# Optimization experiments

Hardware: AMD Instinct MI355X
Metric: run time of the kernel (lower is better)

## Reference

```python
import jax, jax.numpy as jnp
import numpy as np

DIM = 768
H = 12
HD = DIM // H
LAMBDA_INIT = 0.1
EPS = 1e-6


def setup_inputs() -> dict:
    key = jax.random.key(0)
    ks = jax.random.split(key, 6)
    B, N = 2, 2048
    x = jax.random.normal(ks[0], (B, N, DIM), dtype=jnp.float32)
    xpos = jnp.broadcast_to(jnp.arange(N, dtype=jnp.int64), (B, N))
    s = 1.0 / np.sqrt(DIM)
    W_qkv1 = jax.random.normal(ks[1], (DIM, 3 * DIM), dtype=jnp.float32) * s
    W_qkv2 = jax.random.normal(ks[2], (DIM, 3 * DIM), dtype=jnp.float32) * s
    W_proj = jax.random.normal(ks[3], (DIM, DIM), dtype=jnp.float32) * s
    b_proj = jnp.zeros((DIM,), dtype=jnp.float32)
    norm_w = jnp.ones((DIM,), dtype=jnp.float32)
    lambda_1 = jnp.ones((H,), dtype=jnp.float32)
    # layer_idx=0, max_layer=12 -> scale = 1/12
    lambda_2 = jnp.full((H,), 1.0 - LAMBDA_INIT * (1.0 / 12.0), dtype=jnp.float32)
    return {"x": x, "W_qkv1": W_qkv1, "W_qkv2": W_qkv2, "W_proj": W_proj,
            "b_proj": b_proj, "norm_w": norm_w, "lambda_1": lambda_1,
            "lambda_2": lambda_2, "xpos": xpos}


def _qkv(x, W):
    B, N, C = x.shape
    qkv = (x @ W).reshape(B, N, 3, H, HD).transpose(2, 0, 3, 1, 4)  # [3,B,H,N,D]
    return qkv[0], qkv[1], qkv[2]


def reference(x, W_qkv1, W_qkv2, W_proj, b_proj, norm_w, lambda_1, lambda_2, xpos):
    B, N, C = x.shape
    scale = HD ** -0.5
    q1, k1, v1 = _qkv(x, W_qkv1)
    q2, k2, v2 = _qkv(x, W_qkv2)
    attn1 = jax.nn.softmax(jnp.einsum('bhnd,bhmd->bhnm', q1, k1) * scale, axis=-1)
    attn2 = jax.nn.softmax(jnp.einsum('bhnd,bhmd->bhnm', q2, k2) * scale, axis=-1)
    lam = (lambda_1 - lambda_2 + LAMBDA_INIT)[None, :, None, None]
    diff_attn = attn1 - lam * attn2
    out = jnp.einsum('bhnm,bhmd->bhnd', diff_attn, v1)
    out = out.transpose(0, 2, 1, 3).reshape(B, N, C)
    # RMSNorm (computed in fp32, matching torch module)
    o32 = out.astype(jnp.float32)
    rms = jax.lax.rsqrt(jnp.mean(o32 * o32, axis=-1, keepdims=True) + EPS)
    out = (o32 * rms * norm_w).astype(out.dtype)
    return out @ W_proj + b_proj
```

## Files before the change

### kernel.cpp

```cpp
#include <hip/hip_runtime.h>
#include <hip/hip_bf16.h>
#include <math.h>

#define DIMC 768
#define NH   12
#define HDIM 64
#define NSEQ 2048
#define NB   2
#define LAMBDA_INIT 0.1f

typedef __attribute__((ext_vector_type(8))) short bf16x8;
typedef __attribute__((ext_vector_type(4))) float f32x4;
typedef unsigned short u16;

__device__ __forceinline__ u16 f2b(float f) {
    unsigned u = __float_as_uint(f);
    return (u16)((u + 0x7FFFu + ((u >> 16) & 1u)) >> 16);
}
__device__ __forceinline__ float b2f(u16 h) {
    return __uint_as_float((unsigned)h << 16);
}

__global__ __launch_bounds__(256)
void split32(const float* __restrict__ x, u16* __restrict__ hi,
             u16* __restrict__ lo, int n4)
{
    for (int i = blockIdx.x * 256 + threadIdx.x; i < n4; i += gridDim.x * 256) {
        float4 v = ((const float4*)x)[i];
        ushort4 h, l;
        h.x = f2b(v.x); l.x = f2b(v.x - b2f(h.x));
        h.y = f2b(v.y); l.y = f2b(v.y - b2f(h.y));
        h.z = f2b(v.z); l.z = f2b(v.z - b2f(h.z));
        h.w = f2b(v.w); l.w = f2b(v.w - b2f(h.w));
        ((ushort4*)hi)[i] = h;
        ((ushort4*)lo)[i] = l;
    }
}

__global__ __launch_bounds__(256)
void tsplit(const float* __restrict__ src, int R, int C_ld,
            u16* __restrict__ dhi, u16* __restrict__ dlo)
{
    __shared__ float T[64][65];
    const int tid = threadIdx.x;
    const int c0 = blockIdx.x * 64, r0 = blockIdx.y * 64;
    const int row = tid >> 2, cq = (tid & 3) * 4;
#pragma unroll
    for (int it = 0; it < 4; ++it) {
        int col = cq + it * 16;
        float4 v = *(const float4*)&src[(size_t)(r0 + row) * C_ld + c0 + col];
        T[row][col+0] = v.x; T[row][col+1] = v.y;
        T[row][col+2] = v.z; T[row][col+3] = v.w;
    }
    __syncthreads();
    const int c = tid >> 2, rq = (tid & 3) * 4;
#pragma unroll
    for (int it = 0; it < 4; ++it) {
        int rr = rq + it * 16;
#pragma unroll
        for (int i = 0; i < 4; ++i) {
            float f = T[rr + i][c];
            u16 h = f2b(f);
            size_t o = (size_t)(c0 + c) * R + r0 + rr + i;
            dhi[o] = h;
            dlo[o] = f2b(f - b2f(h));
        }
    }
}

template<int MODE>
__global__ __launch_bounds__(256)
void gemm_bf16(const u16* __restrict__ Ahi, const u16* __restrict__ Alo,
               const float* __restrict__ A32,
               const u16* __restrict__ Bhi, const u16* __restrict__ Blo,
               u16* __restrict__ Qo, u16* __restrict__ Ko,
               u16* __restrict__ Vhi, u16* __restrict__ Vlo,
               float* __restrict__ OUT,
               const float* __restrict__ rrms, const float* __restrict__ normw,
               const float* __restrict__ bias)
{
    __shared__ u16 AhS[128][40], AlS[128][40], BhS[128][40], BlS[128][40];
    const int tid = threadIdx.x;
    const int l = tid & 63, w = tid >> 6;
    const int wm = w >> 1, wn = w & 1;
    const int m0 = blockIdx.y * 128, n0 = blockIdx.x * 128;
    const int srow = tid >> 1, scg = (tid & 1) * 16;

    float rsc = 1.0f;
    if (MODE == 2) rsc = rrms[m0 + srow];

    f32x4 acc[4][4];
#pragma unroll
    for (int i = 0; i < 4; ++i)
#pragma unroll
        for (int j = 0; j < 4; ++j) acc[i][j] = (f32x4){0.f,0.f,0.f,0.f};

    for (int k0 = 0; k0 < DIMC; k0 += 32) {
        if (MODE < 2) {
            const u16* pa = Ahi + (size_t)(m0 + srow) * DIMC + k0 + scg;
            const u16* pl = Alo + (size_t)(m0 + srow) * DIMC + k0 + scg;
            *(bf16x8*)&AhS[srow][scg]     = *(const bf16x8*)pa;
            *(bf16x8*)&AhS[srow][scg + 8] = *(const bf16x8*)(pa + 8);
            *(bf16x8*)&AlS[srow][scg]     = *(const bf16x8*)pl;
            *(bf16x8*)&AlS[srow][scg + 8] = *(const bf16x8*)(pl + 8);
        } else {
            const float* pa = A32 + (size_t)(m0 + srow) * DIMC + k0 + scg;
            float4 v0 = *(const float4*)(pa);
            float4 v1 = *(const float4*)(pa + 4);
            float4 v2 = *(const float4*)(pa + 8);
            float4 v3 = *(const float4*)(pa + 12);
            float4 w0 = *(const float4*)(normw + k0 + scg);
            float4 w1 = *(const float4*)(normw + k0 + scg + 4);
            float4 w2 = *(const float4*)(normw + k0 + scg + 8);
            float4 w3 = *(const float4*)(normw + k0 + scg + 12);
            float vv[16] = {v0.x,v0.y,v0.z,v0.w, v1.x,v1.y,v1.z,v1.w,
                            v2.x,v2.y,v2.z,v2.w, v3.x,v3.y,v3.z,v3.w};
            float nn[16] = {w0.x,w0.y,w0.z,w0.w, w1.x,w1.y,w1.z,w1.w,
                            w2.x,w2.y,w2.z,w2.w, w3.x,w3.y,w3.z,w3.w};
#pragma unroll
            for (int i = 0; i < 16; ++i) {
                float f = vv[i] * rsc * nn[i];
                u16 h = f2b(f);
                AhS[srow][scg + i] = h;
                AlS[srow][scg + i] = f2b(f - b2f(h));
            }
        }
        {
            const u16* pb = Bhi + (size_t)(n0 + srow) * DIMC + k0 + scg;
            const u16* pl = Blo + (size_t)(n0 + srow) * DIMC + k0 + scg;
            *(bf16x8*)&BhS[srow][scg]     = *(const bf16x8*)pb;
            *(bf16x8*)&BhS[srow][scg + 8] = *(const bf16x8*)(pb + 8);
            *(bf16x8*)&BlS[srow][scg]     = *(const bf16x8*)pl;
            *(bf16x8*)&BlS[srow][scg + 8] = *(const bf16x8*)(pl + 8);
        }
        __syncthreads();

        bf16x8 ah[4], al[4], bh[4], bl[4];
#pragma unroll
        for (int i = 0; i < 4; ++i) {
            ah[i] = *(const bf16x8*)&AhS[wm*64 + i*16 + (l & 15)][(l >> 4) * 8];
            al[i] = *(const bf16x8*)&AlS[wm*64 + i*16 + (l & 15)][(l >> 4) * 8];
            bh[i] = *(const bf16x8*)&BhS[wn*64 + i*16 + (l & 15)][(l >> 4) * 8];
            bl[i] = *(const bf16x8*)&BlS[wn*64 + i*16 + (l & 15)][(l >> 4) * 8];
        }
#pragma unroll
        for (int mi = 0; mi < 4; ++mi)
#pragma unroll
            for (int ni = 0; ni < 4; ++ni) {
                acc[mi][ni] = __builtin_amdgcn_mfma_f32_16x16x32_bf16(ah[mi], bh[ni], acc[mi][ni], 0, 0, 0);
                acc[mi][ni] = __builtin_amdgcn_mfma_f32_16x16x32_bf16(ah[mi], bl[ni], acc[mi][ni], 0, 0, 0);
                acc[mi][ni] = __builtin_amdgcn_mfma_f32_16x16x32_bf16(al[mi], bh[ni], acc[mi][ni], 0, 0, 0);
            }
        __syncthreads();
    }

#pragma unroll
    for (int mi = 0; mi < 4; ++mi) {
#pragma unroll
        for (int ni = 0; ni < 4; ++ni) {
#pragma unroll
            for (int r = 0; r < 4; ++r) {
                const int m = m0 + wm*64 + mi*16 + (l >> 4) * 4 + r;
                const int n = n0 + wn*64 + ni*16 + (l & 15);
                float val = acc[mi][ni][r];
                if (MODE == 2) {
                    OUT[(size_t)m * DIMC + n] = val + bias[n];
                } else {
                    const int three = n / DIMC;
                    const int rem = n - three * DIMC;
                    const int h = rem >> 6, d = rem & 63;
                    const int b_ = m >> 11, n_ = m & (NSEQ - 1);
                    const size_t o = ((size_t)(b_ * NH + h) * NSEQ + n_) * HDIM + d;
                    if (three == 0)      Qo[o] = f2b(val * 0.125f);
                    else if (three == 1) Ko[o] = f2b(val);
                    else {
                        u16 h16 = f2b(val);
                        Vhi[o] = h16;
                        Vlo[o] = f2b(val - b2f(h16));
                    }
                }
            }
        }
    }
}

#define KVB 64
#define NT  (NSEQ / KVB)

__global__ __launch_bounds__(512)
void attn_mfma4(const u16* __restrict__ Q1, const u16* __restrict__ K1,
                const u16* __restrict__ Vhi, const u16* __restrict__ Vlo,
                const u16* __restrict__ Q2, const u16* __restrict__ K2,
                const float* __restrict__ lam1, const float* __restrict__ lam2,
                float* __restrict__ out)
{
    __shared__ char SMEM[53248];
    u16*      K1s   = (u16*)SMEM;
    u16*      K2s   = (u16*)(SMEM + 8192);
    unsigned* VtHiU = (unsigned*)(SMEM + 16384);
    unsigned* VtLoU = (unsigned*)(SMEM + 25600);
    unsigned* PsU   = (unsigned*)(SMEM + 34816);

    const int tid = threadIdx.x;
    const int l = tid & 63, w = tid >> 6;
    const int branch = w >> 2;
    const int g = w & 3;
    const int qt = blockIdx.x, bh = blockIdx.y;
    const int b = bh / NH, h = bh % NH;
    const size_t hoff = (size_t)bh * NSEQ * HDIM;

    const u16* qbase = branch ? Q2 : Q1;
    const int qrow = qt * 64 + g * 16 + (l & 15);
    const u16* qp = qbase + hoff + (size_t)qrow * HDIM + ((l >> 4) * 8);
    bf16x8 qa[2];
    qa[0] = *(const bf16x8*)(qp);
    qa[1] = *(const bf16x8*)(qp + 32);

    f32x4 o[4];
    float m[4], ls[4];
#pragma unroll
    for (int i = 0; i < 4; ++i) {
        o[i] = (f32x4){0.f,0.f,0.f,0.f};
        m[i] = -INFINITY; ls[i] = 0.f;
    }

    const u16* k1p = K1 + hoff;
    const u16* k2p = K2 + hoff;
    const u16* vhp = Vhi + hoff;
    const u16* vlp = Vlo + hoff;

    const int sr  = tid >> 3;
    const int scu = (tid & 7) * 8;
    const int swz = (sr & 7) << 4;
    const int vp_ = tid & 31;
    const int vdb = (tid >> 5) * 4;

    bf16x8 pk1, pk2;
    ushort4 pvh[2], pvl[2];

#define LOADREGS(KT)                                                           \
    {                                                                          \
        const size_t gk = (size_t)((KT) * KVB + sr) * HDIM + scu;              \
        pk1 = *(const bf16x8*)(k1p + gk);                                      \
        pk2 = *(const bf16x8*)(k2p + gk);                                      \
        const size_t gv = (size_t)((KT) * KVB + 2 * vp_) * HDIM + vdb;         \
        pvh[0] = *(const ushort4*)(vhp + gv);                                  \
        pvh[1] = *(const ushort4*)(vhp + gv + HDIM);                           \
        pvl[0] = *(const ushort4*)(vlp + gv);                                  \
        pvl[1] = *(const ushort4*)(vlp + gv + HDIM);                           \
    }

    LOADREGS(0)

    const char* kb = branch ? (const char*)K2s : (const char*)K1s;
    unsigned* pw = &PsU[w * 576];

    for (int kt = 0; kt < NT; ++kt) {
        __syncthreads();
        *(bf16x8*)((char*)K1s + sr * 128 + ((scu * 2) ^ swz)) = pk1;
        *(bf16x8*)((char*)K2s + sr * 128 + ((scu * 2) ^ swz)) = pk2;
        {
            unsigned hv0[4] = {pvh[0].x, pvh[0].y, pvh[0].z, pvh[0].w};
            unsigned hv1[4] = {pvh[1].x, pvh[1].y, pvh[1].z, pvh[1].w};
            unsigned lv0[4] = {pvl[0].x, pvl[0].y, pvl[0].z, pvl[0].w};
            unsigned lv1[4] = {pvl[1].x, pvl[1].y, pvl[1].z, pvl[1].w};
#pragma unroll
            for (int j = 0; j < 4; ++j) {
                VtHiU[(vdb + j) * 36 + vp_] = hv0[j] | (hv1[j] << 16);
                VtLoU[(vdb + j) * 36 + vp_] = lv0[j] | (lv1[j] << 16);
            }
        }
        __syncthreads();

        if (kt + 1 < NT) LOADREGS(kt + 1)

        f32x4 s[4];
#pragma unroll
        for (int si = 0; si < 4; ++si) s[si] = (f32x4){0.f,0.f,0.f,0.f};
        const int xr = (l & 7) << 4;
#pragma unroll
        for (int hf = 0; hf < 2; ++hf) {
            const int d0b = ((l >> 4) << 4) + (hf << 6);
#pragma unroll
            for (int si = 0; si < 4; ++si) {
                const int ra = si * 16 + (l & 15);
                bf16x8 kv = *(const bf16x8*)(kb + ra * 128 + (d0b ^ xr));
                s[si] = __builtin_amdgcn_mfma_f32_16x16x32_bf16(qa[hf], kv, s[si], 0, 0, 0);
            }
        }

#pragma unroll
        for (int r = 0; r < 4; ++r) {
            const int row = (l >> 4) * 4 + r;
            float rm = fmaxf(fmaxf(s[0][r], s[1][r]), fmaxf(s[2][r], s[3][r]));
#pragma unroll
            for (int mm = 1; mm < 16; mm <<= 1)
                rm = fmaxf(rm, __shfl_xor(rm, mm));
            float mn = fmaxf(m[r], rm);
            float c = __expf(m[r] - mn);
            u16 hh[4];
            float rs = 0.f;
#pragma unroll
            for (int si = 0; si < 4; ++si) {
                hh[si] = f2b(__expf(s[si][r] - mn));
                rs += b2f(hh[si]);
            }
#pragma unroll
            for (int mm = 1; mm < 16; mm <<= 1)
                rs += __shfl_xor(rs, mm);
            ls[r] = ls[r] * c + rs;  m[r] = mn;
#pragma unroll
            for (int dt = 0; dt < 4; ++dt) o[dt][r] *= c;

            int xx[4];
#pragma unroll
            for (int si = 0; si < 4; ++si) xx[si] = __shfl_xor((int)hh[si], 1);
            const int u = l & 15;
            if ((l & 1) == 0) {
                pw[row*36 +      (u >> 1)] = (unsigned)hh[0] | ((unsigned)xx[0] << 16);
                pw[row*36 + 16 + (u >> 1)] = (unsigned)hh[2] | ((unsigned)xx[2] << 16);
            } else {
                pw[row*36 +  8 + (u >> 1)] = (unsigned)xx[1] | ((unsigned)hh[1] << 16);
                pw[row*36 + 24 + (u >> 1)] = (unsigned)xx[3] | ((unsigned)hh[3] << 16);
            }
        }

#pragma unroll
        for (int h2 = 0; h2 < 2; ++h2) {
            const int po = (l & 15) * 144 + h2 * 64 + ((l >> 4) << 4);
            bf16x8 pa = *(const bf16x8*)((const char*)pw + po);
#pragma unroll
            for (int dt = 0; dt < 4; ++dt) {
                const int vo = (dt * 16 + (l & 15)) * 144 + h2 * 64 + ((l >> 4) << 4);
                bf16x8 vhib = *(const bf16x8*)((const char*)VtHiU + vo);
                bf16x8 vlob = *(const bf16x8*)((const char*)VtLoU + vo);
                o[dt] = __builtin_amdgcn_mfma_f32_16x16x32_bf16(pa, vhib, o[dt], 0, 0, 0);
                o[dt] = __builtin_amdgcn_mfma_f32_16x16x32_bf16(pa, vlob, o[dt], 0, 0, 0);
            }
        }
    }
#undef LOADREGS

    __syncthreads();
    float* MRG = (float*)SMEM;
    if (branch == 1) {
        const float lam = lam1[h] - lam2[h] + LAMBDA_INIT;
#pragma unroll
        for (int r = 0; r < 4; ++r) {
            const float i2 = lam / ls[r];
            const int row = (l >> 4) * 4 + r;
#pragma unroll
            for (int dt = 0; dt < 4; ++dt)
                MRG[(g * 16 + row) * 68 + dt * 16 + (l & 15)] = o[dt][r] * i2;
        }
    }
    __syncthreads();
    if (branch == 0) {
#pragma unroll
        for (int r = 0; r < 4; ++r) {
            const float i1 = 1.0f / ls[r];
            const int row = (l >> 4) * 4 + r;
            const int q = qt * 64 + g * 16 + row;
            const size_t rowoff = (size_t)(b * NSEQ + q) * DIMC + h * HDIM;
#pragma unroll
            for (int dt = 0; dt < 4; ++dt)
                out[rowoff + dt * 16 + (l & 15)] =
                    o[dt][r] * i1 - MRG[(g * 16 + row) * 68 + dt * 16 + (l & 15)];
        }
    }
}

__global__ __launch_bounds__(256)
void rrms_kernel(const float* __restrict__ X, float* __restrict__ R)
{
    const int r = blockIdx.x;
    const int t = threadIdx.x;
    const float* row = X + (size_t)r * DIMC;
    float s = 0.f;
#pragma unroll
    for (int k = 0; k < 3; ++k) {
        float v = row[t + k * 256];
        s = fmaf(v, v, s);
    }
#pragma unroll
    for (int mm = 1; mm < 64; mm <<= 1) s += __shfl_xor(s, mm);
    __shared__ float wsum[4];
    if ((t & 63) == 0) wsum[t >> 6] = s;
    __syncthreads();
    if (t == 0) R[r] = rsqrtf((wsum[0]+wsum[1]+wsum[2]+wsum[3]) * (1.0f/DIMC) + 1e-6f);
}

extern "C" void kernel_launch(void* const* d_in, const int* in_sizes, int n_in,
                              void* d_out, int out_size, void* d_ws, size_t ws_size,
                              hipStream_t stream)
{
    const float* x   = (const float*)d_in[0];
    const float* Wq1 = (const float*)d_in[1];
    const float* Wq2 = (const float*)d_in[2];
    const float* Wp  = (const float*)d_in[3];
    const float* bp  = (const float*)d_in[4];
    const float* nw  = (const float*)d_in[5];
    const float* la1 = (const float*)d_in[6];
    const float* la2 = (const float*)d_in[7];
    float* out = (float*)d_out;

    const size_t HSZ = (size_t)NB * NH * NSEQ * HDIM;
    const size_t XSZ = (size_t)NB * NSEQ * DIMC;

    u16* p = (u16*)d_ws;
    u16* Q1b = p;  p += HSZ;
    u16* K1b = p;  p += HSZ;
    u16* Q2b = p;  p += HSZ;
    u16* K2b = p;  p += HSZ;
    u16* V1h = p;  p += HSZ;
    u16* V1l = p;  p += HSZ;
    u16* xhi = p;  p += XSZ;
    u16* xlo = p;  p += XSZ;
    u16* W1th = p; p += (size_t)2304 * 768;
    u16* W1tl = p; p += (size_t)2304 * 768;
    u16* W2th = p; p += (size_t)1536 * 768;
    u16* W2tl = p; p += (size_t)1536 * 768;
    u16* Wpth = p; p += (size_t)768 * 768;
    u16* Wptl = p; p += (size_t)768 * 768;
    float* AO = (float*)p;
    float* RR = AO + XSZ;

    split32<<<dim3(1024), 256, 0, stream>>>(x, xhi, xlo, (int)(XSZ / 4));
    tsplit<<<dim3(36, 12), 256, 0, stream>>>(Wq1, DIMC, 3*DIMC, W1th, W1tl);
    tsplit<<<dim3(24, 12), 256, 0, stream>>>(Wq2, DIMC, 3*DIMC, W2th, W2tl);
    tsplit<<<dim3(12, 12), 256, 0, stream>>>(Wp,  DIMC, DIMC,   Wpth, Wptl);

    gemm_bf16<0><<<dim3(18, 32), 256, 0, stream>>>(xhi, xlo, nullptr, W1th, W1tl,
                                                   Q1b, K1b, V1h, V1l, nullptr,
                                                   nullptr, nullptr, nullptr);
    gemm_bf16<1><<<dim3(12, 32), 256, 0, stream>>>(xhi, xlo, nullptr, W2th, W2tl,
                                                   Q2b, K2b, nullptr, nullptr, nullptr,
                                                   nullptr, nullptr, nullptr);
    attn_mfma4<<<dim3(NSEQ/64, NB*NH), 512, 0, stream>>>(Q1b, K1b, V1h, V1l,
                                                         Q2b, K2b, la1, la2, AO);
    rrms_kernel<<<dim3(NB*NSEQ), 256, 0, stream>>>(AO, RR);
    gemm_bf16<2><<<dim3(6, 32), 256, 0, stream>>>(nullptr, nullptr, AO, Wpth, Wptl,
                                                  nullptr, nullptr, nullptr, nullptr,
                                                  out, RR, nw, bp);
}
```

Baseline: 492.8 us.

## Pre-pack V into transposed tile layout and add lazy softmax rescale with priorities

The QKV GEMM epilogue now writes V hi/lo in a pre-transposed, pair-packed per-tile layout, so the attention kernel loads plain 32-bit words and stores them straight to LDS without repacking. The attention kernel also skips the running-max rescale of the output and sum unless some row's max grows by more than a threshold. It raises wave priority around the MFMA sections. Together these cut address math, global load count and exp/multiply work per KV tile, at the cost of a V layout coupled to the attention tiling and a softmax whose unnormalised exponentials can exceed 1 between rescales.

```diff
diff --git a/kernel.cpp b/kernel.cpp
--- a/kernel.cpp
+++ b/kernel.cpp
@@ -158,25 +158,46 @@
     for (int mi = 0; mi < 4; ++mi) {
 #pragma unroll
         for (int ni = 0; ni < 4; ++ni) {
-#pragma unroll
-            for (int r = 0; r < 4; ++r) {
-                const int m = m0 + wm*64 + mi*16 + (l >> 4) * 4 + r;
-                const int n = n0 + wn*64 + ni*16 + (l & 15);
-                float val = acc[mi][ni][r];
-                if (MODE == 2) {
-                    OUT[(size_t)m * DIMC + n] = val + bias[n];
+            const int n = n0 + wn*64 + ni*16 + (l & 15);
+            const int mbase = m0 + wm*64 + mi*16 + (l >> 4) * 4;
+            if (MODE == 2) {
+#pragma unroll
+                for (int r = 0; r < 4; ++r)
+                    OUT[(size_t)(mbase + r) * DIMC + n] = acc[mi][ni][r] + bias[n];
+            } else {
+                const int three = n / DIMC;
+                const int rem = n - three * DIMC;
+                const int h = rem >> 6, d = rem & 63;
+                if (three == 0) {
+#pragma unroll
+                    for (int r = 0; r < 4; ++r) {
+                        const int m = mbase + r;
+                        const int b_ = m >> 11, n_ = m & (NSEQ - 1);
+                        Qo[((size_t)(b_*NH + h) * NSEQ + n_) * HDIM + d] =
+                            f2b(acc[mi][ni][r] * 0.125f);
+                    }
+                } else if (three == 1) {
+#pragma unroll
+                    for (int r = 0; r < 4; ++r) {
+                        const int m = mbase + r;
+                        const int b_ = m >> 11, n_ = m & (NSEQ - 1);
+                        Ko[((size_t)(b_*NH + h) * NSEQ + n_) * HDIM + d] =
+                            f2b(acc[mi][ni][r]);
+                    }
                 } else {
-                    const int three = n / DIMC;
-                    const int rem = n - three * DIMC;
-                    const int h = rem >> 6, d = rem & 63;
-                    const int b_ = m >> 11, n_ = m & (NSEQ - 1);
-                    const size_t o = ((size_t)(b_ * NH + h) * NSEQ + n_) * HDIM + d;
-                    if (three == 0)      Qo[o] = f2b(val * 0.125f);
-                    else if (three == 1) Ko[o] = f2b(val);
-                    else {
-                        u16 h16 = f2b(val);
-                        Vhi[o] = h16;
-                        Vlo[o] = f2b(val - b2f(h16));
+#pragma unroll
+                    for (int p = 0; p < 2; ++p) {
+                        const float v0 = acc[mi][ni][2*p];
+                        const float v1 = acc[mi][ni][2*p + 1];
+                        const u16 h0 = f2b(v0), h1 = f2b(v1);
+                        const u16 g0 = f2b(v0 - b2f(h0)), g1 = f2b(v1 - b2f(h1));
+                        const int m = mbase + 2*p;
+                        const int b_ = m >> 11, n_ = m & (NSEQ - 1);
+                        const int kt = n_ >> 6, j = (n_ & 63) >> 1;
+                        const size_t o =
+                            (((size_t)(b_*NH + h) * 32 + kt) * 64 + d) * 32 + j;
+                        ((unsigned*)Vhi)[o] = (unsigned)h0 | ((unsigned)h1 << 16);
+                        ((unsigned*)Vlo)[o] = (unsigned)g0 | ((unsigned)g1 << 16);
                     }
                 }
             }
@@ -188,8 +209,8 @@
 #define NT  (NSEQ / KVB)
 
 __global__ __launch_bounds__(512)
-void attn_mfma4(const u16* __restrict__ Q1, const u16* __restrict__ K1,
-                const u16* __restrict__ Vhi, const u16* __restrict__ Vlo,
+void attn_mfma5(const u16* __restrict__ Q1, const u16* __restrict__ K1,
+                const unsigned* __restrict__ VhiP, const unsigned* __restrict__ VloP,
                 const u16* __restrict__ Q2, const u16* __restrict__ K2,
                 const float* __restrict__ lam1, const float* __restrict__ lam2,
                 float* __restrict__ out)
@@ -224,33 +245,30 @@
         m[i] = -INFINITY; ls[i] = 0.f;
     }
 
-    const u16* k1p = K1 + hoff;
-    const u16* k2p = K2 + hoff;
-    const u16* vhp = Vhi + hoff;
-    const u16* vlp = Vlo + hoff;
-
     const int sr  = tid >> 3;
     const int scu = (tid & 7) * 8;
     const int swz = (sr & 7) << 4;
-    const int vp_ = tid & 31;
-    const int vdb = (tid >> 5) * 4;
+    const int vd0 = (tid >> 5) * 4;
+    const int vj  = tid & 31;
+
+    const u16* k1c = K1 + hoff + (size_t)sr * HDIM + scu;
+    const u16* k2c = K2 + hoff + (size_t)sr * HDIM + scu;
+    const unsigned* vhc = VhiP + ((size_t)bh * 32 * 64 + vd0) * 32 + vj;
+    const unsigned* vlc = VloP + ((size_t)bh * 32 * 64 + vd0) * 32 + vj;
 
     bf16x8 pk1, pk2;
-    ushort4 pvh[2], pvl[2];
-
-#define LOADREGS(KT)                                                           \
+    unsigned pvh[4], pvl[4];
+
+#define LOADREGS()                                                             \
     {                                                                          \
-        const size_t gk = (size_t)((KT) * KVB + sr) * HDIM + scu;              \
-        pk1 = *(const bf16x8*)(k1p + gk);                                      \
-        pk2 = *(const bf16x8*)(k2p + gk);                                      \
-        const size_t gv = (size_t)((KT) * KVB + 2 * vp_) * HDIM + vdb;         \
-        pvh[0] = *(const ushort4*)(vhp + gv);                                  \
-        pvh[1] = *(const ushort4*)(vhp + gv + HDIM);                           \
-        pvl[0] = *(const ushort4*)(vlp + gv);                                  \
-        pvl[1] = *(const ushort4*)(vlp + gv + HDIM);                           \
-    }
-
-    LOADREGS(0)
+        pk1 = *(const bf16x8*)k1c;  k1c += KVB * HDIM;                         \
+        pk2 = *(const bf16x8*)k2c;  k2c += KVB * HDIM;                         \
+        pvh[0] = vhc[0];  pvh[1] = vhc[32]; pvh[2] = vhc[64]; pvh[3] = vhc[96];\
+        pvl[0] = vlc[0];  pvl[1] = vlc[32]; pvl[2] = vlc[64]; pvl[3] = vlc[96];\
+        vhc += 64 * 32;  vlc += 64 * 32;                                       \
+    }
+
+    LOADREGS()
 
     const char* kb = branch ? (const char*)K2s : (const char*)K1s;
     unsigned* pw = &PsU[w * 576];
@@ -259,25 +277,20 @@
         __syncthreads();
         *(bf16x8*)((char*)K1s + sr * 128 + ((scu * 2) ^ swz)) = pk1;
         *(bf16x8*)((char*)K2s + sr * 128 + ((scu * 2) ^ swz)) = pk2;
-        {
-            unsigned hv0[4] = {pvh[0].x, pvh[0].y, pvh[0].z, pvh[0].w};
-            unsigned hv1[4] = {pvh[1].x, pvh[1].y, pvh[1].z, pvh[1].w};
-            unsigned lv0[4] = {pvl[0].x, pvl[0].y, pvl[0].z, pvl[0].w};
-            unsigned lv1[4] = {pvl[1].x, pvl[1].y, pvl[1].z, pvl[1].w};
-#pragma unroll
-            for (int j = 0; j < 4; ++j) {
-                VtHiU[(vdb + j) * 36 + vp_] = hv0[j] | (hv1[j] << 16);
-                VtLoU[(vdb + j) * 36 + vp_] = lv0[j] | (lv1[j] << 16);
-            }
+#pragma unroll
+        for (int i = 0; i < 4; ++i) {
+            VtHiU[(vd0 + i) * 36 + vj] = pvh[i];
+            VtLoU[(vd0 + i) * 36 + vj] = pvl[i];
         }
         __syncthreads();
 
-        if (kt + 1 < NT) LOADREGS(kt + 1)
+        if (kt + 1 < NT) LOADREGS()
 
         f32x4 s[4];
 #pragma unroll
         for (int si = 0; si < 4; ++si) s[si] = (f32x4){0.f,0.f,0.f,0.f};
         const int xr = (l & 7) << 4;
+        __builtin_amdgcn_s_setprio(1);
 #pragma unroll
         for (int hf = 0; hf < 2; ++hf) {
             const int d0b = ((l >> 4) << 4) + (hf << 6);
@@ -288,6 +301,7 @@
                 s[si] = __builtin_amdgcn_mfma_f32_16x16x32_bf16(qa[hf], kv, s[si], 0, 0, 0);
             }
         }
+        __builtin_amdgcn_s_setprio(0);
 
 #pragma unroll
         for (int r = 0; r < 4; ++r) {
@@ -296,21 +310,24 @@
 #pragma unroll
             for (int mm = 1; mm < 16; mm <<= 1)
                 rm = fmaxf(rm, __shfl_xor(rm, mm));
-            float mn = fmaxf(m[r], rm);
-            float c = __expf(m[r] - mn);
+            if (__any(rm - m[r] > 8.0f)) {
+                float mn = fmaxf(m[r], rm);
+                float c = __expf(m[r] - mn);
+                ls[r] *= c;  m[r] = mn;
+#pragma unroll
+                for (int dt = 0; dt < 4; ++dt) o[dt][r] *= c;
+            }
             u16 hh[4];
             float rs = 0.f;
 #pragma unroll
             for (int si = 0; si < 4; ++si) {
-                hh[si] = f2b(__expf(s[si][r] - mn));
+                hh[si] = f2b(__expf(s[si][r] - m[r]));
                 rs += b2f(hh[si]);
             }
 #pragma unroll
             for (int mm = 1; mm < 16; mm <<= 1)
                 rs += __shfl_xor(rs, mm);
-            ls[r] = ls[r] * c + rs;  m[r] = mn;
-#pragma unroll
-            for (int dt = 0; dt < 4; ++dt) o[dt][r] *= c;
+            ls[r] += rs;
 
             int xx[4];
 #pragma unroll
@@ -325,6 +342,7 @@
             }
         }
 
+        __builtin_amdgcn_s_setprio(1);
 #pragma unroll
         for (int h2 = 0; h2 < 2; ++h2) {
             const int po = (l & 15) * 144 + h2 * 64 + ((l >> 4) << 4);
@@ -338,6 +356,7 @@
                 o[dt] = __builtin_amdgcn_mfma_f32_16x16x32_bf16(pa, vlob, o[dt], 0, 0, 0);
             }
         }
+        __builtin_amdgcn_s_setprio(0);
     }
 #undef LOADREGS
 
@@ -436,7 +455,9 @@
     gemm_bf16<1><<<dim3(12, 32), 256, 0, stream>>>(xhi, xlo, nullptr, W2th, W2tl,
                                                    Q2b, K2b, nullptr, nullptr, nullptr,
                                                    nullptr, nullptr, nullptr);
-    attn_mfma4<<<dim3(NSEQ/64, NB*NH), 512, 0, stream>>>(Q1b, K1b, V1h, V1l,
+    attn_mfma5<<<dim3(NSEQ/64, NB*NH), 512, 0, stream>>>(Q1b, K1b,
+                                                         (const unsigned*)V1h,
+                                                         (const unsigned*)V1l,
                                                          Q2b, K2b, la1, la2, AO);
     rrms_kernel<<<dim3(NB*NSEQ), 256, 0, stream>>>(AO, RR);
     gemm_bf16<2><<<dim3(6, 32), 256, 0, stream>>>(nullptr, nullptr, AO, Wpth, Wptl,
```

Measured after the change: 599.7 us. 1.22x slower.
